# Optimization experiments

Measured on AMD Instinct MI355X. Metric: run time of the kernel, lower is better.

## Reference

```python
import jax, jax.numpy as jnp
import numpy as np

NORMAL_WEIGHT = 0.001
B, C, N = 8, 6, 4096  # N == n_samples, so no subsampling branch


def setup_inputs() -> dict:
    key = jax.random.key(0)
    k1, k2 = jax.random.split(key)
    a = jax.random.normal(k1, (B, C, N), dtype=jnp.float32)
    b = jax.random.normal(k2, (B, C, N), dtype=jnp.float32)
    return {"a": a, "b": b}


def _chamfer_with_normals(a, b):
    # a, b: [B, 6, N] -> [B, N, 6]
    at = jnp.swapaxes(a, 1, 2)
    bt = jnp.swapaxes(b, 1, 2)
    ap, an = at[:, :, 0:3], at[:, :, 3:6]  # points / normals [B,N,3]
    bp, bn = bt[:, :, 0:3], bt[:, :, 3:6]
    # batch pairwise squared distances: pd[b,i,j] = ||ap_i - bp_j||^2
    aa = jnp.sum(ap * ap, axis=-1)  # [B,N]
    bb = jnp.sum(bp * bp, axis=-1)  # [B,N]
    ab = jnp.einsum('bic,bjc->bij', ap, bp)  # [B,N,N]
    pd = aa[:, :, None] + bb[:, None, :] - 2.0 * ab
    # Faithful to torch: mma[b,i,j]=a_normals[j], mmb[b,i,j]=b_normals[i]
    # so d_norm[b,i,j] = 1 - dot(b_normals[i], a_normals[j])
    d_norm = 1.0 - jnp.einsum('bic,bjc->bij', bn, an)  # [B,N,N]
    d = pd + NORMAL_WEIGHT * d_norm
    chamfer_sym = jnp.sum(jnp.min(d, axis=2)) + jnp.sum(jnp.min(d, axis=1))
    return chamfer_sym / a.shape[0]


def reference(a, b):
    return _chamfer_with_normals(a, b)
```

## Files before the change

### kernel.cpp

```cpp
#include <hip/hip_runtime.h>


constexpr int   NPTS  = 4096;
constexpr int   CPB   = 6;
constexpr int   BATCH = 8;
constexpr float W     = 0.001f;

typedef _Float16 f16x8 __attribute__((ext_vector_type(8)));
typedef float    f32x4 __attribute__((ext_vector_type(4)));

#define MFMA32(A_, B_, C_) __builtin_amdgcn_mfma_f32_16x16x32_f16((A_), (B_), (C_), 0, 0, 0)

__device__ inline void fsplit(float x, _Float16& h, _Float16& l) {
    h = (_Float16)x;
    l = (_Float16)(x - (float)h);
}

__global__ __launch_bounds__(256, 2) void chamfer_fused_kernel(
    const float* __restrict__ A, const float* __restrict__ B,
    float* __restrict__ partial, float* __restrict__ out)
{
    const int dir = blockIdx.z, batch = blockIdx.y, bd = dir * BATCH + batch;
    const int rg = blockIdx.x >> 2, s = blockIdx.x & 3;
    const int tid = threadIdx.x, w = tid >> 6, lane = tid & 63;
    const int quad = lane >> 4, l16 = lane & 15;
    const float* rowPos = dir ? B : A;
    const float* rowNrm = dir ? A : B;
    const float* colPos = dir ? A : B;
    const float* colNrm = dir ? B : A;
    const int bb = batch * CPB * NPTS;
    const _Float16 one = (_Float16)1.f, zz = (_Float16)0.f;

    if (blockIdx.x == 0 && blockIdx.y == 0 && blockIdx.z == 0 && tid == 0)
        out[0] = 0.f;

    __shared__ alignas(16) _Float16 lds[4 * 1024 * 8];

#pragma unroll
    for (int p = 0; p < 4; ++p) {
        const int j  = p * 256 + tid;
        const int cj = s * 1024 + j;
        const float q0 = colPos[bb + 0*NPTS + cj], q1 = colPos[bb + 1*NPTS + cj],
                    q2 = colPos[bb + 2*NPTS + cj];
        const float n0 = colNrm[bb + 3*NPTS + cj], n1 = colNrm[bb + 4*NPTS + cj],
                    n2 = colNrm[bb + 5*NPTS + cj];
        const float c6[6] = {q0, q1, q2, n0, n1, n2};
        const float bias = fmaf(q0, q0, fmaf(q1, q1, q2*q2)) + W;
        _Float16 ch[6], cl[6], bh, bl;
#pragma unroll
        for (int c = 0; c < 6; ++c) fsplit(c6[c], ch[c], cl[c]);
        fsplit(bias, bh, bl);
        f16x8 v0 = {ch[0], ch[1], ch[2], ch[3], ch[4], ch[5], ch[0], ch[1]};
        f16x8 v1 = {ch[2], ch[3], ch[4], ch[5], cl[0], cl[1], cl[2], cl[3]};
        f16x8 v2 = {cl[4], cl[5], cl[0], cl[1], cl[2], cl[3], cl[4], cl[5]};
        f16x8 v3 = {bh, bl, one, one, zz, zz, zz, zz};
        *(f16x8*)&lds[0 * 8192 + j * 8] = v0;
        *(f16x8*)&lds[1 * 8192 + j * 8] = v1;
        *(f16x8*)&lds[2 * 8192 + j * 8] = v2;
        *(f16x8*)&lds[3 * 8192 + j * 8] = v3;
    }

    f16x8 a[8];
#pragma unroll
    for (int rt = 0; rt < 8; ++rt) {
        const int row = rg * 512 + (w * 8 + rt) * 16 + l16;
        const float p0 = rowPos[bb + 0*NPTS + row], p1 = rowPos[bb + 1*NPTS + row],
                    p2 = rowPos[bb + 2*NPTS + row];
        const float rn0 = rowNrm[bb + 3*NPTS + row], rn1 = rowNrm[bb + 4*NPTS + row],
                    rn2 = rowNrm[bb + 5*NPTS + row];
        const float r6[6] = {-2.f*p0, -2.f*p1, -2.f*p2, -W*rn0, -W*rn1, -W*rn2};
        const float aa = fmaf(p0, p0, fmaf(p1, p1, p2*p2));
        _Float16 rh[6], rl[6], ah, al;
#pragma unroll
        for (int c = 0; c < 6; ++c) fsplit(r6[c], rh[c], rl[c]);
        fsplit(aa, ah, al);
        f16x8 af;
        if (quad == 0)      af = f16x8{rh[0], rh[1], rh[2], rh[3], rh[4], rh[5], rl[0], rl[1]};
        else if (quad == 1) af = f16x8{rl[2], rl[3], rl[4], rl[5], rh[0], rh[1], rh[2], rh[3]};
        else if (quad == 2) af = f16x8{rh[4], rh[5], rl[0], rl[1], rl[2], rl[3], rl[4], rl[5]};
        else                af = f16x8{one, one, ah, al, zz, zz, zz, zz};
        a[rt] = af;
    }

    float m[8][4];
#pragma unroll
    for (int rt = 0; rt < 8; ++rt)
#pragma unroll
        for (int r_ = 0; r_ < 4; ++r_) m[rt][r_] = 3.4e38f;

    __syncthreads();

    const _Float16* lq = &lds[quad * 8192];
    const f32x4 z = {0.f, 0.f, 0.f, 0.f};
    for (int ct = 0; ct < 64; ct += 2) {
        const f16x8 b0 = *(const f16x8*)&lq[(ct * 16 + l16) * 8];
        const f16x8 b1 = *(const f16x8*)&lq[((ct + 1) * 16 + l16) * 8];
#pragma unroll
        for (int rt = 0; rt < 8; ++rt) {
            f32x4 acc0 = MFMA32(a[rt], b0, z);
            f32x4 acc1 = MFMA32(a[rt], b1, z);
#pragma unroll
            for (int r_ = 0; r_ < 4; ++r_)
                m[rt][r_] = fminf(m[rt][r_], fminf(acc0[r_], acc1[r_]));
        }
    }

#pragma unroll
    for (int rt = 0; rt < 8; ++rt)
#pragma unroll
        for (int r_ = 0; r_ < 4; ++r_) {
            float v = m[rt][r_];
            v = fminf(v, __shfl_xor(v, 1));
            v = fminf(v, __shfl_xor(v, 2));
            v = fminf(v, __shfl_xor(v, 4));
            v = fminf(v, __shfl_xor(v, 8));
            m[rt][r_] = v;
        }
    if (l16 == 0) {
        float* pb = partial + ((size_t)(s * 16 + bd)) * NPTS + rg * 512;
#pragma unroll
        for (int rt = 0; rt < 8; ++rt) {
            const int rb_ = (w * 8 + rt) * 16 + quad * 4;
            *(float4*)(pb + rb_) = make_float4(m[rt][0], m[rt][1], m[rt][2], m[rt][3]);
        }
    }
}

__global__ __launch_bounds__(256) void reduce_kernel(
    const float* __restrict__ partial, float* __restrict__ out)
{
    const int g = blockIdx.x * 256 + threadIdx.x;
    const int bd = g >> 12, row = g & (NPTS - 1);
    float v = partial[(size_t)(0 * 16 + bd) * NPTS + row];
    v = fminf(v, partial[(size_t)(1 * 16 + bd) * NPTS + row]);
    v = fminf(v, partial[(size_t)(2 * 16 + bd) * NPTS + row]);
    v = fminf(v, partial[(size_t)(3 * 16 + bd) * NPTS + row]);
    for (int off = 32; off; off >>= 1)
        v += __shfl_down(v, off, 64);
    __shared__ float sred[4];
    if ((threadIdx.x & 63) == 0) sred[threadIdx.x >> 6] = v;
    __syncthreads();
    if (threadIdx.x == 0)
        atomicAdd(out, (sred[0] + sred[1] + sred[2] + sred[3]) * 0.125f);
}

extern "C" void kernel_launch(void* const* d_in, const int* in_sizes, int n_in,
                              void* d_out, int out_size, void* d_ws, size_t ws_size,
                              hipStream_t stream) {
    const float* A = (const float*)d_in[0];
    const float* B = (const float*)d_in[1];
    float* out     = (float*)d_out;
    float* partial = (float*)d_ws;

    chamfer_fused_kernel<<<dim3(32, BATCH, 2), 256, 0, stream>>>(A, B, partial, out);
    reduce_kernel<<<dim3(2 * BATCH * NPTS / 256), 256, 0, stream>>>(partial, out);
}
```

Measured before the change: 77.13 us.

## Fuse final reduction into main kernel via last-block atomics; double rows per block

Removes the separate reduce kernel: each block bumps a per-(batch,direction) atomic counter, and the last finishing block computes the min over the column-split partials and sums them, with a second counter finalizing the output. Each wave now covers 16 row tiles instead of 8, so the grid halves to 256 blocks with launch bounds of 1 block per SM, reusing each LDS B-fragment load across more MFMAs. Cross-lane min uses DPP row_ror instead of shuffles. The costs are higher register pressure, fewer blocks (256 on a GPU with many CUs, leaving some idle), and an extra memset launch for the counters.

```diff
diff --git a/kernel.cpp b/kernel.cpp
--- a/kernel.cpp
+++ b/kernel.cpp
@@ -16,9 +16,17 @@
     l = (_Float16)(x - (float)h);
 }
 
-__global__ __launch_bounds__(256, 2) void chamfer_fused_kernel(
+template<int CTRL>
+__device__ inline float minror(float v) {
+    int s = __float_as_int(v);
+    int r = __builtin_amdgcn_update_dpp(s, s, CTRL, 0xF, 0xF, false);
+    return fminf(v, __int_as_float(r));
+}
+
+__global__ __launch_bounds__(256, 1) void chamfer_fused_kernel(
     const float* __restrict__ A, const float* __restrict__ B,
-    float* __restrict__ partial, float* __restrict__ out)
+    float* __restrict__ partial, unsigned* __restrict__ ctrl,
+    float* __restrict__ out)
 {
     const int dir = blockIdx.z, batch = blockIdx.y, bd = dir * BATCH + batch;
     const int rg = blockIdx.x >> 2, s = blockIdx.x & 3;
@@ -30,9 +38,6 @@
     const float* colNrm = dir ? B : A;
     const int bb = batch * CPB * NPTS;
     const _Float16 one = (_Float16)1.f, zz = (_Float16)0.f;
-
-    if (blockIdx.x == 0 && blockIdx.y == 0 && blockIdx.z == 0 && tid == 0)
-        out[0] = 0.f;
 
     __shared__ alignas(16) _Float16 lds[4 * 1024 * 8];
 
@@ -60,10 +65,10 @@
         *(f16x8*)&lds[3 * 8192 + j * 8] = v3;
     }
 
-    f16x8 a[8];
+    f16x8 a[16];
 #pragma unroll
-    for (int rt = 0; rt < 8; ++rt) {
-        const int row = rg * 512 + (w * 8 + rt) * 16 + l16;
+    for (int rt = 0; rt < 16; ++rt) {
+        const int row = rg * 1024 + w * 256 + rt * 16 + l16;
         const float p0 = rowPos[bb + 0*NPTS + row], p1 = rowPos[bb + 1*NPTS + row],
                     p2 = rowPos[bb + 2*NPTS + row];
         const float rn0 = rowNrm[bb + 3*NPTS + row], rn1 = rowNrm[bb + 4*NPTS + row],
@@ -82,9 +87,9 @@
         a[rt] = af;
     }
 
-    float m[8][4];
+    float m[16][4];
 #pragma unroll
-    for (int rt = 0; rt < 8; ++rt)
+    for (int rt = 0; rt < 16; ++rt)
 #pragma unroll
         for (int r_ = 0; r_ < 4; ++r_) m[rt][r_] = 3.4e38f;
 
@@ -92,11 +97,12 @@
 
     const _Float16* lq = &lds[quad * 8192];
     const f32x4 z = {0.f, 0.f, 0.f, 0.f};
+#pragma unroll 2
     for (int ct = 0; ct < 64; ct += 2) {
         const f16x8 b0 = *(const f16x8*)&lq[(ct * 16 + l16) * 8];
         const f16x8 b1 = *(const f16x8*)&lq[((ct + 1) * 16 + l16) * 8];
 #pragma unroll
-        for (int rt = 0; rt < 8; ++rt) {
+        for (int rt = 0; rt < 16; ++rt) {
             f32x4 acc0 = MFMA32(a[rt], b0, z);
             f32x4 acc1 = MFMA32(a[rt], b1, z);
 #pragma unroll
@@ -106,42 +112,62 @@
     }
 
 #pragma unroll
-    for (int rt = 0; rt < 8; ++rt)
+    for (int rt = 0; rt < 16; ++rt)
 #pragma unroll
         for (int r_ = 0; r_ < 4; ++r_) {
             float v = m[rt][r_];
-            v = fminf(v, __shfl_xor(v, 1));
-            v = fminf(v, __shfl_xor(v, 2));
-            v = fminf(v, __shfl_xor(v, 4));
-            v = fminf(v, __shfl_xor(v, 8));
+            v = minror<0x121>(v);
+            v = minror<0x122>(v);
+            v = minror<0x124>(v);
+            v = minror<0x128>(v);
             m[rt][r_] = v;
         }
     if (l16 == 0) {
-        float* pb = partial + ((size_t)(s * 16 + bd)) * NPTS + rg * 512;
+        float* pb = partial + (size_t)(s * 16 + bd) * NPTS + rg * 1024 + w * 256;
 #pragma unroll
-        for (int rt = 0; rt < 8; ++rt) {
-            const int rb_ = (w * 8 + rt) * 16 + quad * 4;
-            *(float4*)(pb + rb_) = make_float4(m[rt][0], m[rt][1], m[rt][2], m[rt][3]);
+        for (int rt = 0; rt < 16; ++rt)
+            *(float4*)(pb + rt * 16 + quad * 4) =
+                make_float4(m[rt][0], m[rt][1], m[rt][2], m[rt][3]);
+    }
+
+    float* sumacc = (float*)(ctrl + 17);
+    __syncthreads();
+    int* flag = (int*)lds;
+    if (tid == 0) {
+        __threadfence();
+        const unsigned old = atomicAdd(&ctrl[bd], 1u);
+        flag[0] = (old == 15u);
+    }
+    __syncthreads();
+    if (!flag[0]) return;
+
+    __threadfence();
+    float mysum = 0.f;
+#pragma unroll
+    for (int i = 0; i < 16; ++i) {
+        const int row = i * 256 + tid;
+        float v = partial[(size_t)(0 * 16 + bd) * NPTS + row];
+        v = fminf(v, partial[(size_t)(1 * 16 + bd) * NPTS + row]);
+        v = fminf(v, partial[(size_t)(2 * 16 + bd) * NPTS + row]);
+        v = fminf(v, partial[(size_t)(3 * 16 + bd) * NPTS + row]);
+        mysum += v;
+    }
+    for (int off = 32; off; off >>= 1)
+        mysum += __shfl_down(mysum, off, 64);
+    __syncthreads();
+    float* sred = (float*)lds;
+    if (lane == 0) sred[w] = mysum;
+    __syncthreads();
+    if (tid == 0) {
+        const float bdsum = sred[0] + sred[1] + sred[2] + sred[3];
+        atomicAdd(sumacc, bdsum);
+        __threadfence();
+        const unsigned old2 = atomicAdd(&ctrl[16], 1u);
+        if (old2 == 15u) {
+            const float total = atomicAdd(sumacc, 0.f);
+            out[0] = total * 0.125f;
         }
     }
-}
-
-__global__ __launch_bounds__(256) void reduce_kernel(
-    const float* __restrict__ partial, float* __restrict__ out)
-{
-    const int g = blockIdx.x * 256 + threadIdx.x;
-    const int bd = g >> 12, row = g & (NPTS - 1);
-    float v = partial[(size_t)(0 * 16 + bd) * NPTS + row];
-    v = fminf(v, partial[(size_t)(1 * 16 + bd) * NPTS + row]);
-    v = fminf(v, partial[(size_t)(2 * 16 + bd) * NPTS + row]);
-    v = fminf(v, partial[(size_t)(3 * 16 + bd) * NPTS + row]);
-    for (int off = 32; off; off >>= 1)
-        v += __shfl_down(v, off, 64);
-    __shared__ float sred[4];
-    if ((threadIdx.x & 63) == 0) sred[threadIdx.x >> 6] = v;
-    __syncthreads();
-    if (threadIdx.x == 0)
-        atomicAdd(out, (sred[0] + sred[1] + sred[2] + sred[3]) * 0.125f);
 }
 
 extern "C" void kernel_launch(void* const* d_in, const int* in_sizes, int n_in,
@@ -150,8 +176,10 @@
     const float* A = (const float*)d_in[0];
     const float* B = (const float*)d_in[1];
     float* out     = (float*)d_out;
-    float* partial = (float*)d_ws;
 
-    chamfer_fused_kernel<<<dim3(32, BATCH, 2), 256, 0, stream>>>(A, B, partial, out);
-    reduce_kernel<<<dim3(2 * BATCH * NPTS / 256), 256, 0, stream>>>(partial, out);
+    float*    partial = (float*)d_ws;
+    unsigned* ctrl    = (unsigned*)((char*)d_ws + (size_t)1024 * 1024);
+
+    hipMemsetAsync(ctrl, 0, 256, stream);
+    chamfer_fused_kernel<<<dim3(16, BATCH, 2), 256, 0, stream>>>(A, B, partial, ctrl, out);
 }
```

Measured after the change: 110.2 us. 1.43x slower.
